# Kernel optimization log

Hardware: AMD Instinct MI355X
Metric: run time of the kernel (lower is better)

Reference implementation:

```python
import jax, jax.numpy as jnp
import numpy as np

NUM_HEADS = 4
CHUNK = 64
GATE_NORM = 16.0
EPS = 1e-5


def _xavier(key, fan_in, fan_out):
    gain = 2.0 ** (-2.5)
    limit = gain * np.sqrt(6.0 / (fan_in + fan_out))
    return jax.random.uniform(key, (fan_in, fan_out), jnp.float32, -limit, limit)


def setup_inputs() -> dict:
    key = jax.random.key(0)
    ks = jax.random.split(key, 8)
    B, L, D = 4, 2048, 1024
    Dk, Dv, R = 1024, 2048, 16
    x = jax.random.normal(ks[0], (B, L, D), jnp.float32)
    return {
        "x": x,
        "Wq": _xavier(ks[1], D, Dk),
        "Wk": _xavier(ks[2], D, Dk),
        "Wv": _xavier(ks[3], D, Dv),
        "Wg": _xavier(ks[4], D, Dv),
        "gk_w1": _xavier(ks[5], D, R),
        "gk_w2": _xavier(ks[6], R, Dk),
        "gk_b2": jnp.zeros((Dk,), jnp.float32),
        "g_norm_w": jnp.ones((Dv // NUM_HEADS,), jnp.float32),
        "Wo": _xavier(ks[7], Dv, D),
    }


def _to_chunks(t, B, H, NC, C):
    # [B,H,L,d] -> [NC,B,H,C,d]
    d = t.shape[-1]
    return t.reshape(B, H, NC, C, d).transpose(2, 0, 1, 3, 4)


def _gla_forward(x, Wq, Wk, Wv, Wg, gk_w1, gk_w2, gk_b2, g_norm_w, Wo):
    B, L, D = x.shape
    H = NUM_HEADS
    C = CHUNK
    NC = L // C

    q = x @ Wq  # [B,L,Dk]
    k = x @ Wk
    v = x @ Wv  # [B,L,Dv]
    gk = jax.nn.log_sigmoid((x @ gk_w1) @ gk_w2 + gk_b2) / GATE_NORM  # [B,L,Dk]

    def split_heads(t):
        return t.reshape(B, L, H, -1).transpose(0, 2, 1, 3)  # [B,H,L,d]

    q, k, v, gk = map(split_heads, (q, k, v, gk))
    dk = q.shape[-1]
    scale = dk ** -0.5

    qc = _to_chunks(q, B, H, NC, C)
    kc = _to_chunks(k, B, H, NC, C)
    vc = _to_chunks(v, B, H, NC, C)
    gc = _to_chunks(gk, B, H, NC, C)
    Bcum = jnp.cumsum(gc, axis=3)  # inclusive log-decay within chunk

    causal = jnp.tril(jnp.ones((C, C), jnp.float32))  # s <= t

    def step(Hst, inp):
        qi, ki, vi, bi = inp  # [B,H,C,dk/dv]
        qg = qi * jnp.exp(bi) * scale           # q_t * exp(B_t)
        kg = ki * jnp.exp(-bi)                  # k_s * exp(-B_s)
        o_inter = jnp.einsum('bhcd,bhde->bhce', qg, Hst)
        A = jnp.einsum('bhtd,bhsd->bhts', qg, kg) * causal
        o_intra = jnp.einsum('bhts,bhse->bhte', A, vi)
        b_last = bi[:, :, -1:, :]               # total chunk decay [B,H,1,dk]
        kH = ki * jnp.exp(b_last - bi)          # decay remaining after s
        H_new = jnp.exp(b_last).transpose(0, 1, 3, 2) * Hst + \
            jnp.einsum('bhcd,bhce->bhde', kH, vi)
        return H_new, o_inter + o_intra

    dv = v.shape[-1]
    H0 = jnp.zeros((B, H, dk, dv), jnp.float32)
    _, oc = jax.lax.scan(step, H0, (qc, kc, vc, Bcum))  # [NC,B,H,C,dv]
    o = oc.transpose(1, 2, 0, 3, 4).reshape(B, H, L, dv)
    o = o.transpose(0, 2, 1, 3)  # [B,L,H,dv]

    # FusedRMSNormSwishGate: RMSNorm(o) * w * swish(g)
    rms = jnp.sqrt(jnp.mean(o * o, axis=-1, keepdims=True) + EPS)
    o_n = (o / rms) * g_norm_w
    g = (x @ Wg).reshape(B, L, H, dv)
    o = o_n * g * jax.nn.sigmoid(g)
    return o.reshape(B, L, H * dv) @ Wo


def reference(x, Wq, Wk, Wv, Wg, gk_w1, gk_w2, gk_b2, g_norm_w, Wo):
    return _gla_forward(x, Wq, Wk, Wv, Wg, gk_w1, gk_w2, gk_b2, g_norm_w, Wo)
```

## Files before the change

kernel.cpp:

```cpp
#include <hip/hip_runtime.h>
#include <hip/hip_bf16.h>

typedef __attribute__((ext_vector_type(8))) __bf16 bf16x8;
typedef __attribute__((ext_vector_type(4))) __bf16 bf16x4;
typedef __attribute__((ext_vector_type(4))) float f32x4;

#define MFMA16(a, b, c) __builtin_amdgcn_mfma_f32_16x16x32_bf16((a), (b), (c), 0, 0, 0)

__device__ __forceinline__ void gload_lds16(const void* g, void* l) {
    __builtin_amdgcn_global_load_lds((const __attribute__((address_space(1))) void*)g,
                                     (__attribute__((address_space(3))) void*)l, 16, 0, 0);
}

__global__ __launch_bounds__(256) void cvt_bf16(const float* __restrict__ in,
                                                __bf16* __restrict__ out, int n4) {
    int i = blockIdx.x * 256 + threadIdx.x;
    if (i >= n4) return;
    f32x4 v = *(const f32x4*)(in + (size_t)i * 4);
    bf16x4 o;
#pragma unroll
    for (int j = 0; j < 4; j++) o[j] = (__bf16)v[j];
    *(bf16x4*)(out + (size_t)i * 4) = o;
}

__global__ __launch_bounds__(256) void transpose_w(const float* __restrict__ in,
                                                   __bf16* __restrict__ out, int R, int C) {
    __shared__ float tile[32][33];
    const int c0 = blockIdx.x * 32, r0 = blockIdx.y * 32;
    const int tx = threadIdx.x, ty = threadIdx.y;
#pragma unroll
    for (int k = 0; k < 32; k += 8)
        tile[ty + k][tx] = in[(size_t)(r0 + ty + k) * C + c0 + tx];
    __syncthreads();
#pragma unroll
    for (int k = 0; k < 32; k += 8)
        out[(size_t)(c0 + ty + k) * R + r0 + tx] = (__bf16)tile[tx][ty + k];
}

template <typename OUT_T>
__global__ __launch_bounds__(256) void gemm_bt(const __bf16* __restrict__ A,
                                               const __bf16* __restrict__ Bt,
                                               OUT_T* __restrict__ C, int M, int N, int K) {
    __shared__ alignas(16) __bf16 As[3][4096];
    __shared__ alignas(16) __bf16 Bs[3][4096];
    const int tid = threadIdx.x;
    const int wv = tid >> 6;
    const int nwg = gridDim.x;
    const int cpx = nwg >> 3;
    const int bid = blockIdx.x;
    const int wg = (bid & 7) * cpx + (bid >> 3);
    const int nbn = N >> 7;
    const int bm = wg / nbn, bn = wg - bm * nbn;

    const __bf16* Ab = A + (size_t)bm * 128 * K;
    const __bf16* Bb = Bt + (size_t)bn * 128 * K;
    const int srow = tid >> 2;
    const int skc = (tid & 3) * 8;
    const int lr = tid & 15;
    const int lk = ((tid >> 4) & 3) * 8;
    const int wm = (wv >> 1) * 64, wn = (wv & 1) * 64;

    auto STAGE = [&](int buf, int kt) {
        gload_lds16(Ab + (size_t)srow * K + kt + skc, &As[buf][0] + wv * 512);
        gload_lds16(Ab + (size_t)(srow + 64) * K + kt + skc, &As[buf][0] + 2048 + wv * 512);
        gload_lds16(Bb + (size_t)srow * K + kt + skc, &Bs[buf][0] + wv * 512);
        gload_lds16(Bb + (size_t)(srow + 64) * K + kt + skc, &Bs[buf][0] + 2048 + wv * 512);
    };

    const int nt = K >> 5;
    STAGE(0, 0);
    STAGE(1, 32);

    f32x4 acc[4][4] = {};
    int buf = 0;
    for (int t = 0; t < nt; ++t) {
        asm volatile("s_waitcnt lgkmcnt(0)" ::: "memory");
        if (t + 1 < nt)
            asm volatile("s_waitcnt vmcnt(4)" ::: "memory");
        else
            asm volatile("s_waitcnt vmcnt(0)" ::: "memory");
        __builtin_amdgcn_s_barrier();
        __builtin_amdgcn_sched_barrier(0);
        if (t + 2 < nt) {
            int nb = buf + 2;
            if (nb >= 3) nb -= 3;
            STAGE(nb, (t + 2) * 32);
        }
        const __bf16* as = &As[buf][0];
        const __bf16* bs = &Bs[buf][0];
        bf16x8 af[4], bfr[4];
#pragma unroll
        for (int i = 0; i < 4; i++) af[i] = *(const bf16x8*)(as + (wm + i * 16 + lr) * 32 + lk);
#pragma unroll
        for (int j = 0; j < 4; j++) bfr[j] = *(const bf16x8*)(bs + (wn + j * 16 + lr) * 32 + lk);
#pragma unroll
        for (int i = 0; i < 4; i++)
#pragma unroll
            for (int j = 0; j < 4; j++) acc[i][j] = MFMA16(af[i], bfr[j], acc[i][j]);
        buf += 1;
        if (buf >= 3) buf -= 3;
    }
    const int lro = ((tid >> 4) & 3) * 4;
#pragma unroll
    for (int i = 0; i < 4; i++)
#pragma unroll
        for (int j = 0; j < 4; j++) {
            size_t base = (size_t)(bm * 128 + wm + i * 16 + lro) * N + bn * 128 + wn + j * 16 + lr;
#pragma unroll
            for (int r = 0; r < 4; r++) C[base + (size_t)r * N] = (OUT_T)acc[i][j][r];
        }
}

__global__ __launch_bounds__(256) void gk1_proj(const float* __restrict__ x,
                                                const float* __restrict__ w1,
                                                float* __restrict__ t) {
    const int row = blockIdx.x * 4 + (threadIdx.x >> 6);
    const int l = threadIdx.x & 63;
    const int r = l & 15, kg = l >> 4;
    const float* xr = x + (size_t)row * 1024;
    const float* w1p = w1 + r;
    float acc = 0.f;
    for (int k = kg * 256; k < (kg + 1) * 256; ++k) acc = fmaf(xr[k], w1p[k * 16], acc);
    acc += __shfl_xor(acc, 16);
    acc += __shfl_xor(acc, 32);
    if (kg == 0) t[(size_t)row * 16 + r] = acc;
}

__global__ __launch_bounds__(1024, 4) void gate_qkg(
    const float* __restrict__ tbuf,
    const float* __restrict__ w2,
    const float* __restrict__ b2,
    const __bf16* __restrict__ qkbuf,
    __bf16* __restrict__ qg,
    __bf16* __restrict__ kg,
    __bf16* __restrict__ kgT,
    float* __restrict__ ebl)
{
    __shared__ alignas(16) float t_l[128 * 16];
    __shared__ float qs[4 * 256];
    __shared__ __bf16 kg_l[128 * 260];
    const int bid = blockIdx.x;
    const int bh = bid & 15, nc = bid >> 4;
    const int b = bh >> 2, h = bh & 3;
    const int tid = threadIdx.x;
    const int d = tid & 255, cq = tid >> 8;
    const int seq0 = b * 2048 + nc * 128;
    const int hd = h * 256 + d;

    for (int i = tid; i < 128 * 16; i += 1024) t_l[i] = tbuf[(size_t)seq0 * 16 + i];
    float w2c[16];
#pragma unroll
    for (int r = 0; r < 16; r++) w2c[r] = w2[r * 1024 + hd];
    const float b2v = b2[hd];
    __syncthreads();

    float bs[32];
    float run = 0.f;
#pragma unroll
    for (int j = 0; j < 32; j++) {
        const int c = cq * 32 + j;
        f32x4 t0 = *(const f32x4*)(t_l + c * 16);
        f32x4 t1 = *(const f32x4*)(t_l + c * 16 + 4);
        f32x4 t2 = *(const f32x4*)(t_l + c * 16 + 8);
        f32x4 t3 = *(const f32x4*)(t_l + c * 16 + 12);
        float u = b2v;
#pragma unroll
        for (int r = 0; r < 4; r++) {
            u = fmaf(t0[r], w2c[r], u);
            u = fmaf(t1[r], w2c[4 + r], u);
            u = fmaf(t2[r], w2c[8 + r], u);
            u = fmaf(t3[r], w2c[12 + r], u);
        }
        const float ls = fminf(u, 0.f) - __logf(1.f + __expf(-fabsf(u)));
        run += ls * 0.0625f;
        bs[j] = run;
    }
    qs[cq * 256 + d] = run;
    __syncthreads();

    float prefix = 0.f;
#pragma unroll
    for (int q = 0; q < 3; q++)
        if (q < cq) prefix += qs[q * 256 + d];

#pragma unroll
    for (int j = 0; j < 32; j++) {
        const int c = cq * 32 + j;
        const float bsum = prefix + bs[j];
        const float eb = __expf(bsum);
        const float en = __expf(-bsum);
        const float qv = (float)qkbuf[(size_t)(seq0 + c) * 2048 + hd];
        const float kv = (float)qkbuf[(size_t)(seq0 + c) * 2048 + 1024 + hd];
        qg[(size_t)(seq0 + c) * 1024 + hd] = (__bf16)(qv * eb * 0.0625f);
        const __bf16 kgv = (__bf16)(kv * en);
        kg[(size_t)(seq0 + c) * 1024 + hd] = kgv;
        kg_l[c * 260 + d] = kgv;
    }
    if (cq == 3) ebl[(size_t)(nc * 16 + bh) * 256 + d] = __expf(prefix + bs[31]);
    __syncthreads();

    {
        const int cc = tid & 127, dgroup = tid >> 7;
        for (int i = 0; i < 32; i++) {
            const int dd = dgroup * 32 + i;
            kgT[(size_t)(bh * 256 + dd) * 2048 + nc * 128 + cc] = kg_l[cc * 260 + dd];
        }
    }
}

__global__ __launch_bounds__(512) void a_mat(
    const __bf16* __restrict__ qg, const __bf16* __restrict__ kg,
    __bf16* __restrict__ Abuf) {
    const int pair = blockIdx.x;
    const int bh = pair & 15, nc = pair >> 4;
    const int b = bh >> 2, h = bh & 3;
    const int tid = threadIdx.x, wv = tid >> 6, l = tid & 63;
    const int lr = l & 15, lk = (l >> 4) * 8, lro = (l >> 4) * 4;
    const int seq0 = b * 2048 + nc * 128;
    __bf16* Ab = Abuf + (size_t)pair * 16384;

    {
        bf16x8 z = {};
        for (int i = tid; i < 2048; i += 512) *(bf16x8*)(Ab + (size_t)i * 8) = z;
    }
    __syncthreads();

    static const int TJ[36] = {0,1,1,2,2,2,3,3,3,3,4,4,4,4,4,5,5,5,5,5,5,
                               6,6,6,6,6,6,6,7,7,7,7,7,7,7,7};
    static const int TS[36] = {0,0,1,0,1,2,0,1,2,3,0,1,2,3,4,0,1,2,3,4,5,
                               0,1,2,3,4,5,6,0,1,2,3,4,5,6,7};
    for (int m = wv; m < 36; m += 8) {
        const int j = TJ[m], s = TS[m];
        f32x4 acc = {};
        const __bf16* qrow = qg + (size_t)(seq0 + j * 16 + lr) * 1024 + h * 256;
        const __bf16* krow = kg + (size_t)(seq0 + s * 16 + lr) * 1024 + h * 256;
#pragma unroll
        for (int ks = 0; ks < 8; ks++) {
            bf16x8 a = *(const bf16x8*)(qrow + ks * 32 + lk);
            bf16x8 bb = *(const bf16x8*)(krow + ks * 32 + lk);
            acc = MFMA16(a, bb, acc);
        }
#pragma unroll
        for (int r = 0; r < 4; r++) {
            const int t = j * 16 + lro + r;
            const int ss = s * 16 + lr;
            if (ss <= t) Ab[t * 128 + ss] = (__bf16)acc[r];
        }
    }
}

__global__ __launch_bounds__(256) void ointer(
    const __bf16* __restrict__ Abuf, const __bf16* __restrict__ qg,
    const __bf16* __restrict__ vt, const __bf16* __restrict__ UH,
    __bf16* __restrict__ ob) {
    __shared__ alignas(16) __bf16 As[4096];
    __shared__ alignas(16) __bf16 Bs[4096];
    const int tid = threadIdx.x;
    const int wv = tid >> 6;
    const int bid = blockIdx.x;
    const int wg = (bid & 7) * 128 + (bid >> 3);
    const int bn = wg & 3, pair = wg >> 2;
    const int bh = pair & 15, nc = pair >> 4;
    const int b = bh >> 2, h = bh & 3;
    const int seq0 = b * 2048 + nc * 128;
    const int srow = tid >> 2;
    const int skc = (tid & 3) * 8;
    const int lr = tid & 15;
    const int lk = ((tid >> 4) & 3) * 8;
    const int wm = (wv >> 1) * 64, wn = (wv & 1) * 64;
    const int KE = (nc == 0) ? 128 : 384;

    const __bf16* Ap = Abuf + (size_t)pair * 16384;
    const __bf16* Hb = UH + ((size_t)((nc - 1) * 16 + bh) * 512 + bn * 128) * 256;

    f32x4 acc[4][4] = {};
    for (int kt = 0; kt < KE; kt += 32) {
        const __bf16 *a0, *a1, *b0, *b1;
        if (kt < 128) {
            a0 = Ap + srow * 128 + kt + skc;
            a1 = Ap + (srow + 64) * 128 + kt + skc;
            b0 = vt + (size_t)(h * 512 + bn * 128 + srow) * 8192 + seq0 + kt + skc;
            b1 = vt + (size_t)(h * 512 + bn * 128 + srow + 64) * 8192 + seq0 + kt + skc;
        } else {
            const int kd = kt - 128;
            a0 = qg + (size_t)(seq0 + srow) * 1024 + h * 256 + kd + skc;
            a1 = qg + (size_t)(seq0 + srow + 64) * 1024 + h * 256 + kd + skc;
            b0 = Hb + (size_t)srow * 256 + kd + skc;
            b1 = Hb + (size_t)(srow + 64) * 256 + kd + skc;
        }
        gload_lds16(a0, As + wv * 512);
        gload_lds16(a1, As + 2048 + wv * 512);
        gload_lds16(b0, Bs + wv * 512);
        gload_lds16(b1, Bs + 2048 + wv * 512);
        asm volatile("s_waitcnt vmcnt(0)" ::: "memory");
        __syncthreads();
        bf16x8 af[4], bfr[4];
#pragma unroll
        for (int i = 0; i < 4; i++) af[i] = *(const bf16x8*)(As + (wm + i * 16 + lr) * 32 + lk);
#pragma unroll
        for (int j = 0; j < 4; j++) bfr[j] = *(const bf16x8*)(Bs + (wn + j * 16 + lr) * 32 + lk);
#pragma unroll
        for (int i = 0; i < 4; i++)
#pragma unroll
            for (int j = 0; j < 4; j++) acc[i][j] = MFMA16(af[i], bfr[j], acc[i][j]);
        __syncthreads();
    }
    const int lro = ((tid >> 4) & 3) * 4;
#pragma unroll
    for (int i = 0; i < 4; i++)
#pragma unroll
        for (int j = 0; j < 4; j++) {
            size_t base = (size_t)(seq0 + wm + i * 16 + lro) * 2048 + h * 512 + bn * 128 + wn + j * 16 + lr;
#pragma unroll
            for (int r = 0; r < 4; r++) ob[base + (size_t)r * 2048] = (__bf16)acc[i][j][r];
        }
}

__global__ __launch_bounds__(512) void chunk_u(
    const __bf16* __restrict__ vt, const __bf16* __restrict__ kgT,
    __bf16* __restrict__ UH) {
    const int bid = blockIdx.x;
    const int bh = bid & 15, nc = (bid >> 4) & 15, q = bid >> 8;
    const int eh = q >> 1, dh = q & 1;
    const int b = bh >> 2, h = bh & 3;
    const int tid = threadIdx.x, wv = tid >> 6, l = tid & 63;
    const int lr = l & 15, lk = (l >> 4) * 8, lro = (l >> 4) * 4;
    const int seq0 = b * 2048 + nc * 128;
    const int e0 = eh * 256 + (wv >> 1) * 64;
    const int d0 = dh * 128 + (wv & 1) * 64;
    const __bf16* va = vt + (size_t)(h * 512 + e0) * 8192 + seq0;
    const __bf16* kb = kgT + (size_t)(bh * 256 + d0) * 2048 + nc * 128;

    f32x4 acc[4][4] = {};
#pragma unroll
    for (int ks = 0; ks < 4; ks++) {
        bf16x8 af[4], bf_[4];
#pragma unroll
        for (int i = 0; i < 4; i++)
            af[i] = *(const bf16x8*)(va + (size_t)(i * 16 + lr) * 8192 + ks * 32 + lk);
#pragma unroll
        for (int j = 0; j < 4; j++)
            bf_[j] = *(const bf16x8*)(kb + (size_t)(j * 16 + lr) * 2048 + ks * 32 + lk);
#pragma unroll
        for (int i = 0; i < 4; i++)
#pragma unroll
            for (int j = 0; j < 4; j++) acc[i][j] = MFMA16(af[i], bf_[j], acc[i][j]);
    }
    __bf16* ub = UH + ((size_t)(nc * 16 + bh) * 512 + e0) * 256 + d0;
#pragma unroll
    for (int i = 0; i < 4; i++)
#pragma unroll
        for (int j = 0; j < 4; j++)
#pragma unroll
            for (int r = 0; r < 4; r++)
                ub[(size_t)(i * 16 + lro + r) * 256 + j * 16 + lr] = (__bf16)acc[i][j][r];
}

__global__ __launch_bounds__(256) void hscan(__bf16* __restrict__ UH,
                                             const float* __restrict__ ebl) {
    const int t = blockIdx.x * 256 + threadIdx.x;
    const int bh = t >> 14;
    const int rem = t & 16383;
    const int e = rem >> 5, d0 = (rem & 31) * 8;
    float H[8];
#pragma unroll
    for (int j = 0; j < 8; j++) H[j] = 0.f;
    for (int i = 0; i < 16; i++) {
        size_t idx = ((size_t)(i * 16 + bh) * 512 + e) * 256 + d0;
        bf16x8 u = *(const bf16x8*)(UH + idx);
        const float* ep = ebl + (size_t)(i * 16 + bh) * 256 + d0;
        f32x4 e0v = *(const f32x4*)ep;
        f32x4 e1v = *(const f32x4*)(ep + 4);
        bf16x8 hw;
#pragma unroll
        for (int j = 0; j < 4; j++) {
            H[j] = e0v[j] * (H[j] + (float)u[j]);
            hw[j] = (__bf16)H[j];
        }
#pragma unroll
        for (int j = 4; j < 8; j++) {
            H[j] = e1v[j - 4] * (H[j] + (float)u[j]);
            hw[j] = (__bf16)H[j];
        }
        *(bf16x8*)(UH + idx) = hw;
    }
}

__global__ __launch_bounds__(256) void rms_gate(const __bf16* __restrict__ ob,
                                                const __bf16* __restrict__ gbuf,
                                                const float* __restrict__ gnw,
                                                __bf16* __restrict__ gated) {
    const int idx = blockIdx.x * 4 + (threadIdx.x >> 6);
    const int seq = idx >> 2, h = idx & 3;
    const int l = threadIdx.x & 63;
    bf16x8 o1 = *(const bf16x8*)(ob + (size_t)seq * 2048 + h * 512 + l * 8);
    float v[8];
    float ms = 0.f;
#pragma unroll
    for (int j = 0; j < 8; j++) {
        v[j] = (float)o1[j];
        ms += v[j] * v[j];
    }
#pragma unroll
    for (int off = 1; off < 64; off <<= 1) ms += __shfl_xor(ms, off);
    const float rinv = rsqrtf(ms * (1.f / 512.f) + 1e-5f);
    bf16x8 gv = *(const bf16x8*)(gbuf + (size_t)seq * 2048 + h * 512 + l * 8);
    const float* gw = gnw + l * 8;
    bf16x8 outv;
#pragma unroll
    for (int j = 0; j < 8; j++) {
        float g = (float)gv[j];
        float sig = 1.f / (1.f + expf(-g));
        outv[j] = (__bf16)(v[j] * rinv * gw[j] * g * sig);
    }
    *(bf16x8*)(gated + (size_t)seq * 2048 + h * 512 + l * 8) = outv;
}

extern "C" void kernel_launch(void* const* d_in, const int* in_sizes, int n_in,
                              void* d_out, int out_size, void* d_ws, size_t ws_size,
                              hipStream_t stream) {
    const float* x = (const float*)d_in[0];
    const float* Wq = (const float*)d_in[1];
    const float* Wk = (const float*)d_in[2];
    const float* Wv = (const float*)d_in[3];
    const float* Wg = (const float*)d_in[4];
    const float* w1 = (const float*)d_in[5];
    const float* w2 = (const float*)d_in[6];
    const float* b2 = (const float*)d_in[7];
    const float* gnw = (const float*)d_in[8];
    const float* Wo = (const float*)d_in[9];
    float* out = (float*)d_out;

    char* p = (char*)d_ws;
    auto nxt = [&](size_t bytes) {
        char* r = p;
        p += (bytes + 255) & ~(size_t)255;
        return r;
    };
    __bf16* xb = (__bf16*)nxt(8192ull * 1024 * 2);
    __bf16* WTqk = (__bf16*)nxt(2048ull * 1024 * 2);
    __bf16* WTg = (__bf16*)nxt(2048ull * 1024 * 2);
    __bf16* WvT = (__bf16*)nxt(2048ull * 1024 * 2);
    __bf16* WoT = (__bf16*)nxt(1024ull * 2048 * 2);
    __bf16* gbuf = (__bf16*)nxt(8192ull * 2048 * 2);
    __bf16* vt = (__bf16*)nxt(2048ull * 8192 * 2);
    float* tbuf = (float*)nxt(8192ull * 16 * 4);
    __bf16* qg = (__bf16*)nxt(8192ull * 1024 * 2);
    __bf16* kgT = (__bf16*)nxt(16ull * 256 * 2048 * 2);
    float* ebl = (float*)nxt(16ull * 16 * 256 * 4);
    __bf16* ob = (__bf16*)nxt(8192ull * 2048 * 2);
    __bf16* UH = (__bf16*)nxt(16ull * 16 * 512 * 256 * 2);
    __bf16* kg = xb;
    __bf16* qkbuf = UH;
    __bf16* gated = UH;
    __bf16* Abuf = WTqk;

    dim3 tb(32, 8);
    cvt_bf16<<<8192, 256, 0, stream>>>(x, xb, 2097152);
    transpose_w<<<dim3(32, 32), tb, 0, stream>>>(Wq, WTqk, 1024, 1024);
    transpose_w<<<dim3(32, 32), tb, 0, stream>>>(Wk, WTqk + 1024 * 1024, 1024, 1024);
    transpose_w<<<dim3(64, 32), tb, 0, stream>>>(Wg, WTg, 1024, 2048);
    transpose_w<<<dim3(64, 32), tb, 0, stream>>>(Wv, WvT, 1024, 2048);
    transpose_w<<<dim3(32, 64), tb, 0, stream>>>(Wo, WoT, 2048, 1024);
    gk1_proj<<<2048, 256, 0, stream>>>(x, w1, tbuf);
    gemm_bt<__bf16><<<1024, 256, 0, stream>>>(xb, WTqk, qkbuf, 8192, 2048, 1024);
    gemm_bt<__bf16><<<1024, 256, 0, stream>>>(xb, WTg, gbuf, 8192, 2048, 1024);
    gemm_bt<__bf16><<<1024, 256, 0, stream>>>(WvT, xb, vt, 2048, 8192, 1024);
    gate_qkg<<<256, 1024, 0, stream>>>(tbuf, w2, b2, qkbuf, qg, kg, kgT, ebl);
    a_mat<<<256, 512, 0, stream>>>(qg, kg, Abuf);
    chunk_u<<<1024, 512, 0, stream>>>(vt, kgT, UH);
    hscan<<<1024, 256, 0, stream>>>(UH, ebl);
    ointer<<<1024, 256, 0, stream>>>(Abuf, qg, vt, UH, ob);
    rms_gate<<<8192, 256, 0, stream>>>(ob, gbuf, gnw, gated);
    gemm_bt<float><<<512, 256, 0, stream>>>(gated, WoT, out, 8192, 1024, 2048);
}
```

Before: 420.2 us.

## Swizzle LDS tiles in GEMMs and triple-buffer the ointer kernel

Adds an XOR swizzle to the LDS layout used by global_load_lds staging in gemm_bt and ointer, remapping which global rows and columns each lane loads so that MFMA fragment reads hit fewer LDS bank conflicts. The ointer kernel also moves from a single-buffered load-wait-compute loop to the same 3-stage pipelined scheme used by gemm_bt, overlapping global loads with MFMA work and dropping one barrier per iteration. This triples ointer's LDS footprint and makes load addressing more complex.

```diff
diff --git a/kernel.cpp b/kernel.cpp
--- a/kernel.cpp
+++ b/kernel.cpp
@@ -10,6 +10,12 @@
 __device__ __forceinline__ void gload_lds16(const void* g, void* l) {
     __builtin_amdgcn_global_load_lds((const __attribute__((address_space(1))) void*)g,
                                      (__attribute__((address_space(3))) void*)l, 16, 0, 0);
+}
+
+__device__ __forceinline__ int lds_swz(int r, int ck) {
+    int W = ((r & 15) << 6) | (ck << 4);
+    W ^= ((W >> 7) & 7) << 4;
+    return ((r >> 4) << 9) + (W >> 1);
 }
 
 __global__ __launch_bounds__(256) void cvt_bf16(const float* __restrict__ in,
@@ -45,6 +51,7 @@
     __shared__ alignas(16) __bf16 Bs[3][4096];
     const int tid = threadIdx.x;
     const int wv = tid >> 6;
+    const int l = tid & 63;
     const int nwg = gridDim.x;
     const int cpx = nwg >> 3;
     const int bid = blockIdx.x;
@@ -54,17 +61,18 @@
 
     const __bf16* Ab = A + (size_t)bm * 128 * K;
     const __bf16* Bb = Bt + (size_t)bn * 128 * K;
-    const int srow = tid >> 2;
-    const int skc = (tid & 3) * 8;
+    const int L = (l << 4) ^ ((l >> 3) << 4);
+    const int sr = L >> 6;
+    const int sc8 = ((L >> 4) & 3) * 8;
     const int lr = tid & 15;
-    const int lk = ((tid >> 4) & 3) * 8;
+    const int ck = (tid >> 4) & 3;
     const int wm = (wv >> 1) * 64, wn = (wv & 1) * 64;
 
     auto STAGE = [&](int buf, int kt) {
-        gload_lds16(Ab + (size_t)srow * K + kt + skc, &As[buf][0] + wv * 512);
-        gload_lds16(Ab + (size_t)(srow + 64) * K + kt + skc, &As[buf][0] + 2048 + wv * 512);
-        gload_lds16(Bb + (size_t)srow * K + kt + skc, &Bs[buf][0] + wv * 512);
-        gload_lds16(Bb + (size_t)(srow + 64) * K + kt + skc, &Bs[buf][0] + 2048 + wv * 512);
+        gload_lds16(Ab + (size_t)(wv * 16 + sr) * K + kt + sc8, &As[buf][0] + wv * 512);
+        gload_lds16(Ab + (size_t)(64 + wv * 16 + sr) * K + kt + sc8, &As[buf][0] + 2048 + wv * 512);
+        gload_lds16(Bb + (size_t)(wv * 16 + sr) * K + kt + sc8, &Bs[buf][0] + wv * 512);
+        gload_lds16(Bb + (size_t)(64 + wv * 16 + sr) * K + kt + sc8, &Bs[buf][0] + 2048 + wv * 512);
     };
 
     const int nt = K >> 5;
@@ -90,9 +98,9 @@
         const __bf16* bs = &Bs[buf][0];
         bf16x8 af[4], bfr[4];
 #pragma unroll
-        for (int i = 0; i < 4; i++) af[i] = *(const bf16x8*)(as + (wm + i * 16 + lr) * 32 + lk);
-#pragma unroll
-        for (int j = 0; j < 4; j++) bfr[j] = *(const bf16x8*)(bs + (wn + j * 16 + lr) * 32 + lk);
+        for (int i = 0; i < 4; i++) af[i] = *(const bf16x8*)(as + lds_swz(wm + i * 16 + lr, ck));
+#pragma unroll
+        for (int j = 0; j < 4; j++) bfr[j] = *(const bf16x8*)(bs + lds_swz(wn + j * 16 + lr, ck));
 #pragma unroll
         for (int i = 0; i < 4; i++)
 #pragma unroll
@@ -253,57 +261,80 @@
     const __bf16* __restrict__ Abuf, const __bf16* __restrict__ qg,
     const __bf16* __restrict__ vt, const __bf16* __restrict__ UH,
     __bf16* __restrict__ ob) {
-    __shared__ alignas(16) __bf16 As[4096];
-    __shared__ alignas(16) __bf16 Bs[4096];
+    __shared__ alignas(16) __bf16 As[3][4096];
+    __shared__ alignas(16) __bf16 Bs[3][4096];
     const int tid = threadIdx.x;
     const int wv = tid >> 6;
+    const int l = tid & 63;
     const int bid = blockIdx.x;
     const int wg = (bid & 7) * 128 + (bid >> 3);
     const int bn = wg & 3, pair = wg >> 2;
     const int bh = pair & 15, nc = pair >> 4;
     const int b = bh >> 2, h = bh & 3;
     const int seq0 = b * 2048 + nc * 128;
-    const int srow = tid >> 2;
-    const int skc = (tid & 3) * 8;
+    const int L = (l << 4) ^ ((l >> 3) << 4);
+    const int sr = L >> 6;
+    const int sc8 = ((L >> 4) & 3) * 8;
     const int lr = tid & 15;
-    const int lk = ((tid >> 4) & 3) * 8;
+    const int ck = (tid >> 4) & 3;
     const int wm = (wv >> 1) * 64, wn = (wv & 1) * 64;
     const int KE = (nc == 0) ? 128 : 384;
 
     const __bf16* Ap = Abuf + (size_t)pair * 16384;
     const __bf16* Hb = UH + ((size_t)((nc - 1) * 16 + bh) * 512 + bn * 128) * 256;
 
-    f32x4 acc[4][4] = {};
-    for (int kt = 0; kt < KE; kt += 32) {
+    auto STAGE = [&](int buf, int kt) {
         const __bf16 *a0, *a1, *b0, *b1;
         if (kt < 128) {
-            a0 = Ap + srow * 128 + kt + skc;
-            a1 = Ap + (srow + 64) * 128 + kt + skc;
-            b0 = vt + (size_t)(h * 512 + bn * 128 + srow) * 8192 + seq0 + kt + skc;
-            b1 = vt + (size_t)(h * 512 + bn * 128 + srow + 64) * 8192 + seq0 + kt + skc;
+            a0 = Ap + (size_t)(wv * 16 + sr) * 128 + kt + sc8;
+            a1 = Ap + (size_t)(64 + wv * 16 + sr) * 128 + kt + sc8;
+            b0 = vt + (size_t)(h * 512 + bn * 128 + wv * 16 + sr) * 8192 + seq0 + kt + sc8;
+            b1 = vt + (size_t)(h * 512 + bn * 128 + 64 + wv * 16 + sr) * 8192 + seq0 + kt + sc8;
         } else {
             const int kd = kt - 128;
-            a0 = qg + (size_t)(seq0 + srow) * 1024 + h * 256 + kd + skc;
-            a1 = qg + (size_t)(seq0 + srow + 64) * 1024 + h * 256 + kd + skc;
-            b0 = Hb + (size_t)srow * 256 + kd + skc;
-            b1 = Hb + (size_t)(srow + 64) * 256 + kd + skc;
-        }
-        gload_lds16(a0, As + wv * 512);
-        gload_lds16(a1, As + 2048 + wv * 512);
-        gload_lds16(b0, Bs + wv * 512);
-        gload_lds16(b1, Bs + 2048 + wv * 512);
-        asm volatile("s_waitcnt vmcnt(0)" ::: "memory");
-        __syncthreads();
+            a0 = qg + (size_t)(seq0 + wv * 16 + sr) * 1024 + h * 256 + kd + sc8;
+            a1 = qg + (size_t)(seq0 + 64 + wv * 16 + sr) * 1024 + h * 256 + kd + sc8;
+            b0 = Hb + (size_t)(wv * 16 + sr) * 256 + kd + sc8;
+            b1 = Hb + (size_t)(64 + wv * 16 + sr) * 256 + kd + sc8;
+        }
+        gload_lds16(a0, &As[buf][0] + wv * 512);
+        gload_lds16(a1, &As[buf][0] + 2048 + wv * 512);
+        gload_lds16(b0, &Bs[buf][0] + wv * 512);
+        gload_lds16(b1, &Bs[buf][0] + 2048 + wv * 512);
+    };
+
+    const int nt = KE >> 5;
+    STAGE(0, 0);
+    STAGE(1, 32);
+
+    f32x4 acc[4][4] = {};
+    int buf = 0;
+    for (int t = 0; t < nt; ++t) {
+        asm volatile("s_waitcnt lgkmcnt(0)" ::: "memory");
+        if (t + 1 < nt)
+            asm volatile("s_waitcnt vmcnt(4)" ::: "memory");
+        else
+            asm volatile("s_waitcnt vmcnt(0)" ::: "memory");
+        __builtin_amdgcn_s_barrier();
+        __builtin_amdgcn_sched_barrier(0);
+        if (t + 2 < nt) {
+            int nb = buf + 2;
+            if (nb >= 3) nb -= 3;
+            STAGE(nb, (t + 2) * 32);
+        }
+        const __bf16* as = &As[buf][0];
+        const __bf16* bs = &Bs[buf][0];
         bf16x8 af[4], bfr[4];
 #pragma unroll
-        for (int i = 0; i < 4; i++) af[i] = *(const bf16x8*)(As + (wm + i * 16 + lr) * 32 + lk);
-#pragma unroll
-        for (int j = 0; j < 4; j++) bfr[j] = *(const bf16x8*)(Bs + (wn + j * 16 + lr) * 32 + lk);
+        for (int i = 0; i < 4; i++) af[i] = *(const bf16x8*)(as + lds_swz(wm + i * 16 + lr, ck));
+#pragma unroll
+        for (int j = 0; j < 4; j++) bfr[j] = *(const bf16x8*)(bs + lds_swz(wn + j * 16 + lr, ck));
 #pragma unroll
         for (int i = 0; i < 4; i++)
 #pragma unroll
             for (int j = 0; j < 4; j++) acc[i][j] = MFMA16(af[i], bfr[j], acc[i][j]);
-        __syncthreads();
+        buf += 1;
+        if (buf >= 3) buf -= 3;
     }
     const int lro = ((tid >> 4) & 3) * 4;
 #pragma unroll
```

New measurement: 414.0 us. Within noise of the previous version (-1.5%).
